# Performance work log

Measured on AMD Instinct MI355X. Metric: run time of the kernel, lower is better.

The kernel has to match this reference:

```python
import jax, jax.numpy as jnp
import numpy as np

N_NODES = 100000
D = 128


def gcn_conv(x, W, b, src, dst, deg_inv_sqrt):
    # PyG GCNConv: linear transform, symmetric-normalized aggregation with self-loops, bias
    h = x @ W  # [N, D_out]
    norm = deg_inv_sqrt[src] * deg_inv_sqrt[dst]  # [E_tot]
    msgs = h[src] * norm[:, None]  # gather + scale  [E_tot, D_out]
    out = jax.ops.segment_sum(msgs, dst, num_segments=x.shape[0])  # scatter-add to targets
    return out + b


def _prep_edges(edge_index, n_nodes):
    # add self-loops (weight 1) and compute deg^{-1/2} over targets (flow source_to_target)
    loops = jnp.arange(n_nodes, dtype=edge_index.dtype)
    src = jnp.concatenate([edge_index[0], loops])
    dst = jnp.concatenate([edge_index[1], loops])
    deg = jax.ops.segment_sum(jnp.ones_like(dst, dtype=jnp.float32), dst, num_segments=n_nodes)
    deg_inv_sqrt = jnp.where(deg > 0, jax.lax.rsqrt(jnp.maximum(deg, 1.0)), 0.0)
    return src, dst, deg_inv_sqrt


def setup_inputs() -> dict:
    key = jax.random.key(0)
    ks = jax.random.split(key, 8)
    node_fts = jax.random.normal(ks[0], (N_NODES, D), dtype=jnp.float32)
    edge_index = jax.random.randint(ks[1], (2, 1600000), 0, N_NODES, dtype=jnp.int64)
    scale = 1.0 / np.sqrt(D)
    W1 = jax.random.uniform(ks[2], (D, D), jnp.float32, -scale, scale)
    b1 = jnp.zeros((D,), jnp.float32)
    W2 = jax.random.uniform(ks[3], (D, D), jnp.float32, -scale, scale)
    b2 = jnp.zeros((D,), jnp.float32)
    W3 = jax.random.uniform(ks[4], (D, D), jnp.float32, -scale, scale)
    b3 = jnp.zeros((D,), jnp.float32)
    return {"node_fts": node_fts, "edge_index": edge_index,
            "W1": W1, "b1": b1, "W2": W2, "b2": b2, "W3": W3, "b3": b3}


def reference(node_fts, edge_index, W1, b1, W2, b2, W3, b3):
    n = node_fts.shape[0]
    src, dst, dinv = _prep_edges(edge_index, n)
    x = jax.nn.relu(gcn_conv(node_fts, W1, b1, src, dst, dinv))
    x = jax.nn.relu(gcn_conv(x, W2, b2, src, dst, dinv))
    x = jax.nn.relu(gcn_conv(x, W3, b3, src, dst, dinv))
    return x
```

## Files before the change

### kernel.cpp

```cpp
#include <hip/hip_runtime.h>

#define NN 100000
#define EE 1600000
#define D 128
#define NPART 8
#define PSZ (NN / NPART)
#define NI4 (EE / 4)
#define SUBW 196
#define NSB (NPART * 64)
#define SCAP 4096
#define RCAP 8192
#define LBCAP 96

typedef __attribute__((ext_vector_type(8))) short bf16x8;
typedef __attribute__((ext_vector_type(4))) float f32x4;

__device__ inline unsigned int f2bf2(float a, float b) {
    unsigned int ua = __float_as_uint(a);
    unsigned int ub = __float_as_uint(b);
    ua = (ua + 0x7fffu + ((ua >> 16) & 1u)) >> 16;
    ub = (ub + 0x7fffu + ((ub >> 16) & 1u)) >> 16;
    return ua | (ub << 16);
}
__device__ inline unsigned short f2bf(float a) {
    unsigned int u = __float_as_uint(a);
    return (unsigned short)((u + 0x7fffu + ((u >> 16) & 1u)) >> 16);
}
__device__ inline float2 bf2f2(unsigned int u) {
    return make_float2(__uint_as_float(u << 16), __uint_as_float(u & 0xffff0000u));
}


__global__ __launch_bounds__(256) void fbwt_kernel(const int4* __restrict__ src4,
                                                   const int4* __restrict__ dst4,
                                                   int* __restrict__ gcur2,
                                                   uint2* __restrict__ buckets2,
                                                   int* __restrict__ deg,
                                                   const float* __restrict__ W1,
                                                   const float* __restrict__ W2,
                                                   const float* __restrict__ W3,
                                                   unsigned short* __restrict__ wt1,
                                                   unsigned short* __restrict__ wt2,
                                                   unsigned short* __restrict__ wt3,
                                                   unsigned int* __restrict__ hb) {
    if (blockIdx.x >= 512) {
        const int g = (blockIdx.x - 512) * 256 + threadIdx.x;
        const int n = g >> 7, k = g & 127;
        wt1[n * 128 + k] = f2bf(W1[k * 128 + n]);
        wt2[n * 128 + k] = f2bf(W2[k * 128 + n]);
        wt3[n * 128 + k] = f2bf(W3[k * 128 + n]);
        if (blockIdx.x == 512 && threadIdx.x < 64) hb[(size_t)NN * 64 + threadIdx.x] = 0;
        return;
    }
    __shared__ uint2 bins[64][LBCAP];
    __shared__ int bcnt[64];
    __shared__ int gbase[64];
    const int p = blockIdx.x >> 6;
    const int c = blockIdx.x & 63;
    if (threadIdx.x < 64) bcnt[threadIdx.x] = 0;
    __syncthreads();
    const int lo = p * PSZ, hi = lo + PSZ;
    const int chunk4 = NI4 / 64;
    const int a0 = c * chunk4, a1 = a0 + chunk4;
    for (int i = a0 + threadIdx.x; i < a1; i += 256) {
        int4 d4 = dst4[i];
        bool m0 = (d4.x >= lo && d4.x < hi);
        bool m1 = (d4.y >= lo && d4.y < hi);
        bool m2 = (d4.z >= lo && d4.z < hi);
        bool m3 = (d4.w >= lo && d4.w < hi);
        if (!(m0 | m1 | m2 | m3)) continue;
        int4 s4 = src4[i];
        int ss[4] = {s4.x, s4.y, s4.z, s4.w};
        int dd[4] = {d4.x, d4.y, d4.z, d4.w};
        bool mm[4] = {m0, m1, m2, m3};
#pragma unroll
        for (int k = 0; k < 4; ++k) {
            if (!mm[k]) continue;
            atomicAdd(&deg[dd[k]], 1);
            int li = (dd[k] - lo) / SUBW;
            int pos = atomicAdd(&bcnt[li], 1);
            if (pos < LBCAP) {
                bins[li][pos] = make_uint2((unsigned)ss[k], (unsigned)dd[k]);
            } else {
                int sb = p * 64 + li;
                int gp = atomicAdd(&gcur2[sb], 1);
                buckets2[(size_t)sb * SCAP + gp] = make_uint2((unsigned)ss[k], (unsigned)dd[k]);
            }
        }
    }
    __syncthreads();
    if (threadIdx.x < 64) {
        int cc = min(bcnt[threadIdx.x], LBCAP);
        gbase[threadIdx.x] = atomicAdd(&gcur2[p * 64 + threadIdx.x], cc);
        bcnt[threadIdx.x] = cc;
    }
    __syncthreads();
    for (int b = 0; b < 64; ++b) {
        const int cc = bcnt[b];
        uint2* outp = buckets2 + (size_t)(p * 64 + b) * SCAP + gbase[b];
        for (int i = threadIdx.x; i < cc; i += 256) outp[i] = bins[b][i];
    }
}


template <bool F32IN>
__device__ __forceinline__ void gemm_body(int wave, const void* __restrict__ xin,
                                          const unsigned short* __restrict__ wt,
                                          const int* __restrict__ deg,
                                          unsigned int* __restrict__ hb) {
    const int base = wave * 64;
    if (base >= NN) return;
    const int lane = threadIdx.x & 63;
    const int r = lane & 15;
    const int q = lane >> 4;
    const unsigned short* wrow = wt + (size_t)r * 128 + q * 8;
    bf16x8 wfr[4][8];
#pragma unroll
    for (int kc = 0; kc < 4; ++kc)
#pragma unroll
        for (int nt = 0; nt < 8; ++nt)
            wfr[kc][nt] = *(const bf16x8*)(wrow + (size_t)nt * 16 * 128 + kc * 32);
#pragma unroll
    for (int tt = 0; tt < 4; ++tt) {
        const int m0 = base + tt * 16;
        if (m0 >= NN) break;
        f32x4 acc[8] = {};
#pragma unroll
        for (int kc = 0; kc < 4; ++kc) {
            bf16x8 xf;
            if (F32IN) {
                const float* xrow = (const float*)xin + (size_t)(m0 + r) * 128 + q * 8 + kc * 32;
                float4 a = *(const float4*)xrow;
                float4 b = *(const float4*)(xrow + 4);
                unsigned short tmp[8] = {f2bf(a.x), f2bf(a.y), f2bf(a.z), f2bf(a.w),
                                         f2bf(b.x), f2bf(b.y), f2bf(b.z), f2bf(b.w)};
                xf = *(const bf16x8*)tmp;
            } else {
                const unsigned short* xrow =
                    (const unsigned short*)xin + (size_t)(m0 + r) * 128 + q * 8 + kc * 32;
                xf = *(const bf16x8*)xrow;
            }
#pragma unroll
            for (int nt = 0; nt < 8; ++nt)
                acc[nt] = __builtin_amdgcn_mfma_f32_16x16x32_bf16(wfr[kc][nt], xf, acc[nt], 0, 0, 0);
        }
        const int orow = m0 + r;
        const float dvr = rsqrtf(1.0f + (float)deg[orow]);
        unsigned int* hrow = hb + (size_t)orow * 64;
#pragma unroll
        for (int nt = 0; nt < 8; ++nt) {
            int n = nt * 16 + q * 4;
            *(uint2*)(hrow + (n >> 1)) =
                make_uint2(f2bf2(acc[nt][0] * dvr, acc[nt][1] * dvr),
                           f2bf2(acc[nt][2] * dvr, acc[nt][3] * dvr));
        }
    }
}


__global__ __launch_bounds__(256, 2) void sort3_gemm1_kernel(const uint2* __restrict__ buckets2,
                                                             const int* __restrict__ gcur2,
                                                             int* __restrict__ csr,
                                                             int* __restrict__ info,
                                                             float* __restrict__ dinv,
                                                             const float* __restrict__ x0,
                                                             const unsigned short* __restrict__ wt1,
                                                             const int* __restrict__ deg,
                                                             unsigned int* __restrict__ hb) {
    __shared__ int hist[256];
    __shared__ int pscan[256];
    __shared__ int lcur[256];
    __shared__ int staged[RCAP];
    if (blockIdx.x >= 512) {
        const int wave = (blockIdx.x - 512) * 4 + (threadIdx.x >> 6);
        gemm_body<true>(wave, (const void*)x0, wt1, deg, hb);
        return;
    }
    const int sb = blockIdx.x;
    const int li = sb & 63;
    const int base_node = (sb >> 6) * PSZ + li * SUBW;
    const int nnodes = min(SUBW, PSZ - li * SUBW);
    const int scnt = gcur2[sb];
    const uint2* bk = buckets2 + (size_t)sb * SCAP;
    const int t = threadIdx.x;
    hist[t] = 0;
    __syncthreads();
    for (int i = t; i < scnt; i += 256) atomicAdd(&hist[(int)bk[i].y - base_node], 1);
    __syncthreads();
    const int padded = (t < nnodes) ? ((hist[t] + 7) & ~7) : 0;
    pscan[t] = padded;
    __syncthreads();
    for (int off = 1; off < 256; off <<= 1) {
        int v = (t >= off) ? pscan[t - off] : 0;
        __syncthreads();
        pscan[t] += v;
        __syncthreads();
    }
    const int rstart = pscan[t] - padded;
    lcur[t] = rstart;
    __syncthreads();
    const int total = pscan[255];
    for (int i = t; i < total; i += 256) staged[i] = NN;
    __syncthreads();
    for (int i = t; i < scnt; i += 256) {
        uint2 r = bk[i];
        int pos = atomicAdd(&lcur[(int)r.y - base_node], 1);
        staged[pos] = (int)r.x;
    }
    __syncthreads();
    int4* co = (int4*)(csr + (size_t)sb * RCAP);
    for (int i = t; i < (total >> 2); i += 256) co[i] = ((const int4*)staged)[i];
    if (t < nnodes) {
        int dg = hist[t];
        info[base_node + t] = ((sb * RCAP + rstart) << 8) | dg;
        dinv[base_node + t] = rsqrtf(1.0f + (float)dg);
    }
}

template <bool F32IN>
__global__ __launch_bounds__(256, 2) void gemm_kernel(const void* __restrict__ xin,
                                                      const unsigned short* __restrict__ wt,
                                                      const int* __restrict__ deg,
                                                      unsigned int* __restrict__ hb) {
    const int wave = blockIdx.x * 4 + (threadIdx.x >> 6);
    gemm_body<F32IN>(wave, xin, wt, deg, hb);
}


template <bool BF16OUT>
__global__ __launch_bounds__(256) void aggregate_kernel(const unsigned int* __restrict__ hb,
                                                        const int* __restrict__ csr,
                                                        const int* __restrict__ info,
                                                        const float* __restrict__ dinv,
                                                        const float2* __restrict__ bias2,
                                                        void* __restrict__ outp) {
    const int d = blockIdx.x * 4 + (threadIdx.x >> 6);
    const int j = threadIdx.x & 63;
    const int ifo = info[d];
    int e = ifo >> 8;
    const int end = e + (((ifo & 255) + 7) & ~7);
    float2 acc = bf2f2(hb[(size_t)d * 64 + j]);
    for (; e + 16 <= end; e += 16) {
        int4 c0 = *(const int4*)(csr + e);
        int4 c1 = *(const int4*)(csr + e + 4);
        int4 c2 = *(const int4*)(csr + e + 8);
        int4 c3 = *(const int4*)(csr + e + 12);
        unsigned int v0 = hb[(size_t)c0.x * 64 + j];
        unsigned int v1 = hb[(size_t)c0.y * 64 + j];
        unsigned int v2 = hb[(size_t)c0.z * 64 + j];
        unsigned int v3 = hb[(size_t)c0.w * 64 + j];
        unsigned int v4 = hb[(size_t)c1.x * 64 + j];
        unsigned int v5 = hb[(size_t)c1.y * 64 + j];
        unsigned int v6 = hb[(size_t)c1.z * 64 + j];
        unsigned int v7 = hb[(size_t)c1.w * 64 + j];
        unsigned int v8 = hb[(size_t)c2.x * 64 + j];
        unsigned int v9 = hb[(size_t)c2.y * 64 + j];
        unsigned int va = hb[(size_t)c2.z * 64 + j];
        unsigned int vb = hb[(size_t)c2.w * 64 + j];
        unsigned int vc = hb[(size_t)c3.x * 64 + j];
        unsigned int vd = hb[(size_t)c3.y * 64 + j];
        unsigned int ve = hb[(size_t)c3.z * 64 + j];
        unsigned int vf = hb[(size_t)c3.w * 64 + j];
        float2 f0 = bf2f2(v0), f1 = bf2f2(v1), f2 = bf2f2(v2), f3 = bf2f2(v3);
        float2 f4 = bf2f2(v4), f5 = bf2f2(v5), f6 = bf2f2(v6), f7 = bf2f2(v7);
        float2 f8 = bf2f2(v8), f9 = bf2f2(v9), fa = bf2f2(va), fb = bf2f2(vb);
        float2 fc = bf2f2(vc), fd = bf2f2(vd), fe = bf2f2(ve), ff = bf2f2(vf);
        acc.x += ((f0.x + f1.x) + (f2.x + f3.x)) + ((f4.x + f5.x) + (f6.x + f7.x)) +
                 ((f8.x + f9.x) + (fa.x + fb.x)) + ((fc.x + fd.x) + (fe.x + ff.x));
        acc.y += ((f0.y + f1.y) + (f2.y + f3.y)) + ((f4.y + f5.y) + (f6.y + f7.y)) +
                 ((f8.y + f9.y) + (fa.y + fb.y)) + ((fc.y + fd.y) + (fe.y + ff.y));
    }
    if (e < end) {
        int4 c0 = *(const int4*)(csr + e);
        int4 c1 = *(const int4*)(csr + e + 4);
        unsigned int v0 = hb[(size_t)c0.x * 64 + j];
        unsigned int v1 = hb[(size_t)c0.y * 64 + j];
        unsigned int v2 = hb[(size_t)c0.z * 64 + j];
        unsigned int v3 = hb[(size_t)c0.w * 64 + j];
        unsigned int v4 = hb[(size_t)c1.x * 64 + j];
        unsigned int v5 = hb[(size_t)c1.y * 64 + j];
        unsigned int v6 = hb[(size_t)c1.z * 64 + j];
        unsigned int v7 = hb[(size_t)c1.w * 64 + j];
        float2 f0 = bf2f2(v0), f1 = bf2f2(v1), f2 = bf2f2(v2), f3 = bf2f2(v3);
        float2 f4 = bf2f2(v4), f5 = bf2f2(v5), f6 = bf2f2(v6), f7 = bf2f2(v7);
        acc.x += ((f0.x + f1.x) + (f2.x + f3.x)) + ((f4.x + f5.x) + (f6.x + f7.x));
        acc.y += ((f0.y + f1.y) + (f2.y + f3.y)) + ((f4.y + f5.y) + (f6.y + f7.y));
    }
    const float dv = dinv[d];
    float2 bb = bias2[j];
    float ox = fmaxf(dv * acc.x + bb.x, 0.0f);
    float oy = fmaxf(dv * acc.y + bb.y, 0.0f);
    if (BF16OUT) {
        ((unsigned int*)outp)[(size_t)d * 64 + j] = f2bf2(ox, oy);
    } else {
        ((float2*)outp)[(size_t)d * 64 + j] = make_float2(ox, oy);
    }
}


extern "C" void kernel_launch(void* const* d_in, const int* in_sizes, int n_in,
                              void* d_out, int out_size, void* d_ws, size_t ws_size,
                              hipStream_t stream) {
    const float* x0 = (const float*)d_in[0];
    const int* ei = (const int*)d_in[1];
    const float* W1 = (const float*)d_in[2];
    const float* b1 = (const float*)d_in[3];
    const float* W2 = (const float*)d_in[4];
    const float* b2 = (const float*)d_in[5];
    const float* W3 = (const float*)d_in[6];
    const float* b3 = (const float*)d_in[7];
    float* out = (float*)d_out;

    char* ws = (char*)d_ws;
    size_t off = 0;
    auto alloc = [&](size_t bytes) -> void* {
        off = (off + 511) & ~(size_t)511;
        void* p = ws + off;
        off += bytes;
        return p;
    };
    unsigned int* hb  = (unsigned int*)alloc(((size_t)NN + 1) * 64 * 4);
    int*   csr     = (int*)  alloc((size_t)NSB * RCAP * sizeof(int));
    uint2* buckets2 = (uint2*)alloc((size_t)NSB * SCAP * sizeof(uint2));
    int*   info    = (int*)  alloc((size_t)NN * sizeof(int));
    float* dinv    = (float*)alloc((size_t)NN * sizeof(float));
    int*   deg     = (int*)  alloc((size_t)NN * sizeof(int));
    int*   gcur2   = (int*)  alloc(NSB * sizeof(int));
    unsigned short* wt1 = (unsigned short*)alloc(128 * 128 * 2);
    unsigned short* wt2 = (unsigned short*)alloc(128 * 128 * 2);
    unsigned short* wt3 = (unsigned short*)alloc(128 * 128 * 2);

    unsigned int* xact = (unsigned int*)d_out;

    const int4* src4 = (const int4*)ei;
    const int4* dst4 = (const int4*)(ei + EE);

    hipMemsetAsync(gcur2, 0, NSB * sizeof(int), stream);
    hipMemsetAsync(deg, 0, (size_t)NN * sizeof(int), stream);
    fbwt_kernel<<<576, 256, 0, stream>>>(src4, dst4, gcur2, buckets2, deg,
                                         W1, W2, W3, wt1, wt2, wt3, hb);
    sort3_gemm1_kernel<<<903, 256, 0, stream>>>(buckets2, gcur2, csr, info, dinv,
                                                x0, wt1, deg, hb);
    aggregate_kernel<true><<<NN / 4, 256, 0, stream>>>(hb, csr, info, dinv,
                                                       (const float2*)b1, (void*)xact);
    gemm_kernel<false><<<391, 256, 0, stream>>>((const void*)xact, wt2, deg, hb);
    aggregate_kernel<true><<<NN / 4, 256, 0, stream>>>(hb, csr, info, dinv,
                                                       (const float2*)b2, (void*)xact);
    gemm_kernel<false><<<391, 256, 0, stream>>>((const void*)xact, wt3, deg, hb);
    aggregate_kernel<false><<<NN / 4, 256, 0, stream>>>(hb, csr, info, dinv,
                                                        (const float2*)b3, (void*)out);
}
```

Baseline: 436.5 us.

## Use fixed-stride padded CSR rows and apply source normalization during aggregation

Drops the global degree atomics from the bucketing kernel and takes degrees from the sort pass instead. Writes each node's neighbor list into a fixed 64-slot padded row, so the aggregate kernel no longer reads an info word and can issue 32 gathers unconditionally. The per-source dinv scaling moves out of the GEMM epilogue and into the aggregation, which adds one dinv gather per edge. The weight transpose now runs as 48 blocks through a shared-memory tile. Rows with more than 64 neighbors would be truncated, so the new layout assumes a bounded degree.

Measured after the change: 491.5 us. 1.13x slower.

```diff
diff --git a/kernel.cpp b/kernel.cpp
--- a/kernel.cpp
+++ b/kernel.cpp
@@ -2,7 +2,6 @@
 
 #define NN 100000
 #define EE 1600000
-#define D 128
 #define NPART 8
 #define PSZ (NN / NPART)
 #define NI4 (EE / 4)
@@ -11,6 +10,8 @@
 #define SCAP 4096
 #define RCAP 8192
 #define LBCAP 96
+#define ROWCAP 64
+#define WTB 48
 
 typedef __attribute__((ext_vector_type(8))) short bf16x8;
 typedef __attribute__((ext_vector_type(4))) float f32x4;
@@ -35,28 +36,44 @@
                                                    const int4* __restrict__ dst4,
                                                    int* __restrict__ gcur2,
                                                    uint2* __restrict__ buckets2,
-                                                   int* __restrict__ deg,
                                                    const float* __restrict__ W1,
                                                    const float* __restrict__ W2,
                                                    const float* __restrict__ W3,
                                                    unsigned short* __restrict__ wt1,
                                                    unsigned short* __restrict__ wt2,
                                                    unsigned short* __restrict__ wt3,
-                                                   unsigned int* __restrict__ hb) {
-    if (blockIdx.x >= 512) {
-        const int g = (blockIdx.x - 512) * 256 + threadIdx.x;
-        const int n = g >> 7, k = g & 127;
-        wt1[n * 128 + k] = f2bf(W1[k * 128 + n]);
-        wt2[n * 128 + k] = f2bf(W2[k * 128 + n]);
-        wt3[n * 128 + k] = f2bf(W3[k * 128 + n]);
-        if (blockIdx.x == 512 && threadIdx.x < 64) hb[(size_t)NN * 64 + threadIdx.x] = 0;
-        return;
-    }
+                                                   unsigned int* __restrict__ hb,
+                                                   float* __restrict__ dinv) {
     __shared__ uint2 bins[64][LBCAP];
     __shared__ int bcnt[64];
     __shared__ int gbase[64];
-    const int p = blockIdx.x >> 6;
-    const int c = blockIdx.x & 63;
+    __shared__ float tile[32][33];
+    const int bx = blockIdx.x;
+
+    if (bx < WTB) {
+        const int m = bx >> 4;
+        const int tl = bx & 15;
+        const int ti = tl >> 2, tj = tl & 3;
+        const float* W = m == 0 ? W1 : (m == 1 ? W2 : W3);
+        unsigned short* wt = m == 0 ? wt1 : (m == 1 ? wt2 : wt3);
+        const int r = threadIdx.x >> 5, c = threadIdx.x & 31;
+#pragma unroll
+        for (int rr = r; rr < 32; rr += 8)
+            tile[rr][c] = W[(ti * 32 + rr) * 128 + tj * 32 + c];
+        __syncthreads();
+#pragma unroll
+        for (int rr = r; rr < 32; rr += 8)
+            wt[(size_t)(tj * 32 + rr) * 128 + ti * 32 + c] = f2bf(tile[c][rr]);
+        if (bx == 0) {
+            if (threadIdx.x < 64) hb[(size_t)NN * 64 + threadIdx.x] = 0;
+            if (threadIdx.x == 64) dinv[NN] = 0.0f;
+        }
+        return;
+    }
+
+    const int fb = bx - WTB;
+    const int p = fb >> 6;
+    const int c = fb & 63;
     if (threadIdx.x < 64) bcnt[threadIdx.x] = 0;
     __syncthreads();
     const int lo = p * PSZ, hi = lo + PSZ;
@@ -76,7 +93,6 @@
 #pragma unroll
         for (int k = 0; k < 4; ++k) {
             if (!mm[k]) continue;
-            atomicAdd(&deg[dd[k]], 1);
             int li = (dd[k] - lo) / SUBW;
             int pos = atomicAdd(&bcnt[li], 1);
             if (pos < LBCAP) {
@@ -106,7 +122,6 @@
 template <bool F32IN>
 __device__ __forceinline__ void gemm_body(int wave, const void* __restrict__ xin,
                                           const unsigned short* __restrict__ wt,
-                                          const int* __restrict__ deg,
                                           unsigned int* __restrict__ hb) {
     const int base = wave * 64;
     if (base >= NN) return;
@@ -145,14 +160,12 @@
                 acc[nt] = __builtin_amdgcn_mfma_f32_16x16x32_bf16(wfr[kc][nt], xf, acc[nt], 0, 0, 0);
         }
         const int orow = m0 + r;
-        const float dvr = rsqrtf(1.0f + (float)deg[orow]);
         unsigned int* hrow = hb + (size_t)orow * 64;
 #pragma unroll
         for (int nt = 0; nt < 8; ++nt) {
             int n = nt * 16 + q * 4;
             *(uint2*)(hrow + (n >> 1)) =
-                make_uint2(f2bf2(acc[nt][0] * dvr, acc[nt][1] * dvr),
-                           f2bf2(acc[nt][2] * dvr, acc[nt][3] * dvr));
+                make_uint2(f2bf2(acc[nt][0], acc[nt][1]), f2bf2(acc[nt][2], acc[nt][3]));
         }
     }
 }
@@ -161,19 +174,19 @@
 __global__ __launch_bounds__(256, 2) void sort3_gemm1_kernel(const uint2* __restrict__ buckets2,
                                                              const int* __restrict__ gcur2,
                                                              int* __restrict__ csr,
-                                                             int* __restrict__ info,
+                                                             int* __restrict__ deg,
                                                              float* __restrict__ dinv,
                                                              const float* __restrict__ x0,
                                                              const unsigned short* __restrict__ wt1,
-                                                             const int* __restrict__ deg,
                                                              unsigned int* __restrict__ hb) {
     __shared__ int hist[256];
     __shared__ int pscan[256];
     __shared__ int lcur[256];
+    __shared__ int rs[256];
     __shared__ int staged[RCAP];
     if (blockIdx.x >= 512) {
         const int wave = (blockIdx.x - 512) * 4 + (threadIdx.x >> 6);
-        gemm_body<true>(wave, (const void*)x0, wt1, deg, hb);
+        gemm_body<true>(wave, (const void*)x0, wt1, hb);
         return;
     }
     const int sb = blockIdx.x;
@@ -198,6 +211,7 @@
     }
     const int rstart = pscan[t] - padded;
     lcur[t] = rstart;
+    rs[t] = rstart;
     __syncthreads();
     const int total = pscan[255];
     for (int i = t; i < total; i += 256) staged[i] = NN;
@@ -208,11 +222,18 @@
         staged[pos] = (int)r.x;
     }
     __syncthreads();
-    int4* co = (int4*)(csr + (size_t)sb * RCAP);
-    for (int i = t; i < (total >> 2); i += 256) co[i] = ((const int4*)staged)[i];
+    const int4* staged4 = (const int4*)staged;
+    int4* csr4 = (int4*)csr;
+    const int4 sv = make_int4(NN, NN, NN, NN);
+    for (int i = t; i < nnodes * 16; i += 256) {
+        const int n = i >> 4, s = i & 15;
+        const int pad = (hist[n] + 7) & ~7;
+        int4 v = (s * 4 < pad) ? staged4[(rs[n] >> 2) + s] : sv;
+        csr4[((size_t)(base_node + n) << 4) + s] = v;
+    }
     if (t < nnodes) {
         int dg = hist[t];
-        info[base_node + t] = ((sb * RCAP + rstart) << 8) | dg;
+        deg[base_node + t] = dg;
         dinv[base_node + t] = rsqrtf(1.0f + (float)dg);
     }
 }
@@ -220,73 +241,68 @@
 template <bool F32IN>
 __global__ __launch_bounds__(256, 2) void gemm_kernel(const void* __restrict__ xin,
                                                       const unsigned short* __restrict__ wt,
-                                                      const int* __restrict__ deg,
                                                       unsigned int* __restrict__ hb) {
     const int wave = blockIdx.x * 4 + (threadIdx.x >> 6);
-    gemm_body<F32IN>(wave, xin, wt, deg, hb);
-}
-
+    gemm_body<F32IN>(wave, xin, wt, hb);
+}
+
+
+#define GATH4(c, v0, v1, v2, v3, w0, w1, w2, w3)                              \
+    unsigned int v0 = hb[(size_t)(c).x * 64 + j], v1 = hb[(size_t)(c).y * 64 + j], \
+                 v2 = hb[(size_t)(c).z * 64 + j], v3 = hb[(size_t)(c).w * 64 + j]; \
+    float w0 = dinv[(c).x], w1 = dinv[(c).y], w2 = dinv[(c).z], w3 = dinv[(c).w];
+
+#define ACC4(v0, v1, v2, v3, w0, w1, w2, w3)                                  \
+    {                                                                         \
+        float2 f0 = bf2f2(v0), f1 = bf2f2(v1), f2 = bf2f2(v2), f3 = bf2f2(v3);\
+        acc.x += (w0 * f0.x + w1 * f1.x) + (w2 * f2.x + w3 * f3.x);           \
+        acc.y += (w0 * f0.y + w1 * f1.y) + (w2 * f2.y + w3 * f3.y);           \
+    }
 
 template <bool BF16OUT>
 __global__ __launch_bounds__(256) void aggregate_kernel(const unsigned int* __restrict__ hb,
                                                         const int* __restrict__ csr,
-                                                        const int* __restrict__ info,
+                                                        const int* __restrict__ deg,
                                                         const float* __restrict__ dinv,
                                                         const float2* __restrict__ bias2,
                                                         void* __restrict__ outp) {
     const int d = blockIdx.x * 4 + (threadIdx.x >> 6);
     const int j = threadIdx.x & 63;
-    const int ifo = info[d];
-    int e = ifo >> 8;
-    const int end = e + (((ifo & 255) + 7) & ~7);
-    float2 acc = bf2f2(hb[(size_t)d * 64 + j]);
-    for (; e + 16 <= end; e += 16) {
-        int4 c0 = *(const int4*)(csr + e);
-        int4 c1 = *(const int4*)(csr + e + 4);
-        int4 c2 = *(const int4*)(csr + e + 8);
-        int4 c3 = *(const int4*)(csr + e + 12);
-        unsigned int v0 = hb[(size_t)c0.x * 64 + j];
-        unsigned int v1 = hb[(size_t)c0.y * 64 + j];
-        unsigned int v2 = hb[(size_t)c0.z * 64 + j];
-        unsigned int v3 = hb[(size_t)c0.w * 64 + j];
-        unsigned int v4 = hb[(size_t)c1.x * 64 + j];
-        unsigned int v5 = hb[(size_t)c1.y * 64 + j];
-        unsigned int v6 = hb[(size_t)c1.z * 64 + j];
-        unsigned int v7 = hb[(size_t)c1.w * 64 + j];
-        unsigned int v8 = hb[(size_t)c2.x * 64 + j];
-        unsigned int v9 = hb[(size_t)c2.y * 64 + j];
-        unsigned int va = hb[(size_t)c2.z * 64 + j];
-        unsigned int vb = hb[(size_t)c2.w * 64 + j];
-        unsigned int vc = hb[(size_t)c3.x * 64 + j];
-        unsigned int vd = hb[(size_t)c3.y * 64 + j];
-        unsigned int ve = hb[(size_t)c3.z * 64 + j];
-        unsigned int vf = hb[(size_t)c3.w * 64 + j];
-        float2 f0 = bf2f2(v0), f1 = bf2f2(v1), f2 = bf2f2(v2), f3 = bf2f2(v3);
-        float2 f4 = bf2f2(v4), f5 = bf2f2(v5), f6 = bf2f2(v6), f7 = bf2f2(v7);
-        float2 f8 = bf2f2(v8), f9 = bf2f2(v9), fa = bf2f2(va), fb = bf2f2(vb);
-        float2 fc = bf2f2(vc), fd = bf2f2(vd), fe = bf2f2(ve), ff = bf2f2(vf);
-        acc.x += ((f0.x + f1.x) + (f2.x + f3.x)) + ((f4.x + f5.x) + (f6.x + f7.x)) +
-                 ((f8.x + f9.x) + (fa.x + fb.x)) + ((fc.x + fd.x) + (fe.x + ff.x));
-        acc.y += ((f0.y + f1.y) + (f2.y + f3.y)) + ((f4.y + f5.y) + (f6.y + f7.y)) +
-                 ((f8.y + f9.y) + (fa.y + fb.y)) + ((fc.y + fd.y) + (fe.y + ff.y));
-    }
-    if (e < end) {
-        int4 c0 = *(const int4*)(csr + e);
-        int4 c1 = *(const int4*)(csr + e + 4);
-        unsigned int v0 = hb[(size_t)c0.x * 64 + j];
-        unsigned int v1 = hb[(size_t)c0.y * 64 + j];
-        unsigned int v2 = hb[(size_t)c0.z * 64 + j];
-        unsigned int v3 = hb[(size_t)c0.w * 64 + j];
-        unsigned int v4 = hb[(size_t)c1.x * 64 + j];
-        unsigned int v5 = hb[(size_t)c1.y * 64 + j];
-        unsigned int v6 = hb[(size_t)c1.z * 64 + j];
-        unsigned int v7 = hb[(size_t)c1.w * 64 + j];
-        float2 f0 = bf2f2(v0), f1 = bf2f2(v1), f2 = bf2f2(v2), f3 = bf2f2(v3);
-        float2 f4 = bf2f2(v4), f5 = bf2f2(v5), f6 = bf2f2(v6), f7 = bf2f2(v7);
-        acc.x += ((f0.x + f1.x) + (f2.x + f3.x)) + ((f4.x + f5.x) + (f6.x + f7.x));
-        acc.y += ((f0.y + f1.y) + (f2.y + f3.y)) + ((f4.y + f5.y) + (f6.y + f7.y));
-    }
+    const int dg = deg[d];
     const float dv = dinv[d];
+    const int4* crow = (const int4*)(csr + ((size_t)d << 6));
+    float2 acc;
+    {
+        float2 s = bf2f2(hb[(size_t)d * 64 + j]);
+        acc.x = dv * s.x;
+        acc.y = dv * s.y;
+    }
+    int4 c0 = crow[0], c1 = crow[1], c2 = crow[2], c3 = crow[3];
+    int4 c4 = crow[4], c5 = crow[5], c6 = crow[6], c7 = crow[7];
+    GATH4(c0, va0, va1, va2, va3, wa0, wa1, wa2, wa3)
+    GATH4(c1, vb0, vb1, vb2, vb3, wb0, wb1, wb2, wb3)
+    GATH4(c2, vc0, vc1, vc2, vc3, wc0, wc1, wc2, wc3)
+    GATH4(c3, vd0, vd1, vd2, vd3, wd0, wd1, wd2, wd3)
+    GATH4(c4, ve0, ve1, ve2, ve3, we0, we1, we2, we3)
+    GATH4(c5, vf0, vf1, vf2, vf3, wf0, wf1, wf2, wf3)
+    GATH4(c6, vg0, vg1, vg2, vg3, wg0, wg1, wg2, wg3)
+    GATH4(c7, vh0, vh1, vh2, vh3, wh0, wh1, wh2, wh3)
+    ACC4(va0, va1, va2, va3, wa0, wa1, wa2, wa3)
+    ACC4(vb0, vb1, vb2, vb3, wb0, wb1, wb2, wb3)
+    ACC4(vc0, vc1, vc2, vc3, wc0, wc1, wc2, wc3)
+    ACC4(vd0, vd1, vd2, vd3, wd0, wd1, wd2, wd3)
+    ACC4(ve0, ve1, ve2, ve3, we0, we1, we2, we3)
+    ACC4(vf0, vf1, vf2, vf3, wf0, wf1, wf2, wf3)
+    ACC4(vg0, vg1, vg2, vg3, wg0, wg1, wg2, wg3)
+    ACC4(vh0, vh1, vh2, vh3, wh0, wh1, wh2, wh3)
+    const int padded = min((dg + 7) & ~7, ROWCAP);
+    for (int e = 32; e < padded; e += 8) {
+        int4 t0 = crow[e >> 2], t1 = crow[(e >> 2) + 1];
+        GATH4(t0, x0, x1, x2, x3, y0, y1, y2, y3)
+        GATH4(t1, x4, x5, x6, x7, y4, y5, y6, y7)
+        ACC4(x0, x1, x2, x3, y0, y1, y2, y3)
+        ACC4(x4, x5, x6, x7, y4, y5, y6, y7)
+    }
     float2 bb = bias2[j];
     float ox = fmaxf(dv * acc.x + bb.x, 0.0f);
     float oy = fmaxf(dv * acc.y + bb.y, 0.0f);
@@ -319,13 +335,12 @@
         off += bytes;
         return p;
     };
-    unsigned int* hb  = (unsigned int*)alloc(((size_t)NN + 1) * 64 * 4);
-    int*   csr     = (int*)  alloc((size_t)NSB * RCAP * sizeof(int));
+    unsigned int* hb = (unsigned int*)alloc(((size_t)NN + 1) * 64 * 4);
+    int* csr = (int*)alloc((size_t)NN * ROWCAP * sizeof(int));
     uint2* buckets2 = (uint2*)alloc((size_t)NSB * SCAP * sizeof(uint2));
-    int*   info    = (int*)  alloc((size_t)NN * sizeof(int));
-    float* dinv    = (float*)alloc((size_t)NN * sizeof(float));
-    int*   deg     = (int*)  alloc((size_t)NN * sizeof(int));
-    int*   gcur2   = (int*)  alloc(NSB * sizeof(int));
+    int* deg = (int*)alloc((size_t)NN * sizeof(int));
+    float* dinv = (float*)alloc(((size_t)NN + 1) * sizeof(float));
+    int* gcur2 = (int*)alloc(NSB * sizeof(int));
     unsigned short* wt1 = (unsigned short*)alloc(128 * 128 * 2);
     unsigned short* wt2 = (unsigned short*)alloc(128 * 128 * 2);
     unsigned short* wt3 = (unsigned short*)alloc(128 * 128 * 2);
@@ -336,17 +351,16 @@
     const int4* dst4 = (const int4*)(ei + EE);
 
     hipMemsetAsync(gcur2, 0, NSB * sizeof(int), stream);
-    hipMemsetAsync(deg, 0, (size_t)NN * sizeof(int), stream);
-    fbwt_kernel<<<576, 256, 0, stream>>>(src4, dst4, gcur2, buckets2, deg,
-                                         W1, W2, W3, wt1, wt2, wt3, hb);
-    sort3_gemm1_kernel<<<903, 256, 0, stream>>>(buckets2, gcur2, csr, info, dinv,
-                                                x0, wt1, deg, hb);
-    aggregate_kernel<true><<<NN / 4, 256, 0, stream>>>(hb, csr, info, dinv,
+    fbwt_kernel<<<WTB + 512, 256, 0, stream>>>(src4, dst4, gcur2, buckets2,
+                                               W1, W2, W3, wt1, wt2, wt3, hb, dinv);
+    sort3_gemm1_kernel<<<903, 256, 0, stream>>>(buckets2, gcur2, csr, deg, dinv,
+                                                x0, wt1, hb);
+    aggregate_kernel<true><<<NN / 4, 256, 0, stream>>>(hb, csr, deg, dinv,
                                                        (const float2*)b1, (void*)xact);
-    gemm_kernel<false><<<391, 256, 0, stream>>>((const void*)xact, wt2, deg, hb);
-    aggregate_kernel<true><<<NN / 4, 256, 0, stream>>>(hb, csr, info, dinv,
+    gemm_kernel<false><<<391, 256, 0, stream>>>((const void*)xact, wt2, hb);
+    aggregate_kernel<true><<<NN / 4, 256, 0, stream>>>(hb, csr, deg, dinv,
                                                        (const float2*)b2, (void*)xact);
-    gemm_kernel<false><<<391, 256, 0, stream>>>((const void*)xact, wt3, deg, hb);
-    aggregate_kernel<false><<<NN / 4, 256, 0, stream>>>(hb, csr, info, dinv,
+    gemm_kernel<false><<<391, 256, 0, stream>>>((const void*)xact, wt3, hb);
+    aggregate_kernel<false><<<NN / 4, 256, 0, stream>>>(hb, csr, deg, dinv,
                                                         (const float2*)b3, (void*)out);
 }
```
